# Kernel tuning notes

Measured on AMD Instinct MI355X. Metric: run time of the kernel, lower is better.

The kernel has to match this reference:

```python
import jax, jax.numpy as jnp
from jax import lax
import numpy as np

B, N, C = 16, 8192, 256


def farthest_point_sample(pts, npoint):
    # pts: [B, N, 3]. Standard PointNet++ FPS; is_center=True -> start from the
    # point farthest from the centroid (argmax of dist-to-mean).
    b, n, _ = pts.shape
    centroid = pts.mean(axis=1, keepdims=True)                  # [B,1,3]
    d0 = jnp.sum((pts - centroid) ** 2, axis=-1)                # [B,N]
    farthest = jnp.argmax(d0, axis=-1)                          # [B]
    dist = jnp.full((b, n), 1e10, dtype=pts.dtype)

    def step(carry, _):
        dist, far = carry
        cur = jnp.take_along_axis(pts, far[:, None, None], axis=1)  # [B,1,3]
        d = jnp.sum((pts - cur) ** 2, axis=-1)                      # [B,N]
        dist = jnp.minimum(dist, d)
        new_far = jnp.argmax(dist, axis=-1)
        return (dist, new_far), far

    (_, _), idxs = lax.scan(step, (dist, farthest), None, length=npoint)
    return idxs.T  # [B, npoint]


def index_points(x, idx):
    # x: [B, N, D], idx: [B, M] -> [B, M, D]
    return jnp.take_along_axis(x, idx[:, :, None], axis=1)


def setup_inputs() -> dict:
    key = jax.random.key(0)
    k1, k2 = jax.random.split(key)
    points = jax.random.normal(k1, (B, 3, N), dtype=jnp.float32)
    features = jax.random.normal(k2, (B, C, N), dtype=jnp.float32)
    return {"points": points, "features": features, "num_points": 2048}


def reference(points, features, num_points):
    pts = jnp.swapaxes(points, -1, -2)     # [B,N,3]
    feats = jnp.swapaxes(features, -1, -2) # [B,N,C]
    idx = farthest_point_sample(pts, num_points)  # [B,M] int
    sampled_points = index_points(pts, idx)       # [B,M,3]
    sampled_features = index_points(feats, idx)   # [B,M,C]
    return sampled_points, sampled_features
```

## Files before the change

### kernel.cpp

```cpp
#include <hip/hip_runtime.h>
#include <cfloat>

#define BB 16
#define NN 8192
#define CC 256
#define NT 256
#define PPT 32
#define NPAIR (PPT / 2)
#define NWAVES (NT / 64)
#define TIT (1024 / NT)
#define TBLOCKS 240
#define NTILES (BB * (CC / 64) * (NN / 64))

typedef float    v2f __attribute__((ext_vector_type(2)));
typedef unsigned v2u __attribute__((ext_vector_type(2)));
typedef unsigned uu;
typedef unsigned long long ull;

#define LDS_BARRIER() __asm__ __volatile__("s_waitcnt lgkmcnt(0)\n\ts_barrier" ::: "memory")

struct SmemFPS {
  float px[NN], py[NN], pz[NN];
  ull   key[2][NWAVES];
  float red[NWAVES][3];
  float ctr[3];
};
struct SmemT {
  float tile[64][65];
};
union Smem { SmemFPS f; SmemT t; };

__device__ __forceinline__ v2f pk_sub(v2f a, v2f b) {
  v2f d;
  asm("v_pk_add_f32 %0, %1, %2 neg_lo:[0,1] neg_hi:[0,1]"
      : "=v"(d) : "v"(a), "v"(b));
  return d;
}
__device__ __forceinline__ v2f pk_mul(v2f a, v2f b) {
  v2f d;
  asm("v_pk_mul_f32 %0, %1, %2" : "=v"(d) : "v"(a), "v"(b));
  return d;
}
__device__ __forceinline__ v2f pk_add(v2f a, v2f b) {
  v2f d;
  asm("v_pk_add_f32 %0, %1, %2" : "=v"(d) : "v"(a), "v"(b));
  return d;
}

__device__ __forceinline__ uu umin2(uu a, uu b) { return a < b ? a : b; }
__device__ __forceinline__ uu umax2(uu a, uu b) { return a > b ? a : b; }

__device__ __forceinline__ ull max64(ull a, ull b) { return a > b ? a : b; }

template <int CTRL>
__device__ __forceinline__ ull dpp_max64(ull x) {
  int lo = (int)(uu)x;
  int hi = (int)(uu)(x >> 32);
  int plo = __builtin_amdgcn_update_dpp(0, lo, CTRL, 0xF, 0xF, true);
  int phi = __builtin_amdgcn_update_dpp(0, hi, CTRL, 0xF, 0xF, true);
  ull p = ((ull)(uu)phi << 32) | (uu)plo;
  return max64(x, p);
}

__device__ __forceinline__ ull wave_max63(ull k) {
  k = dpp_max64<0xB1>(k);
  k = dpp_max64<0x4E>(k);
  k = dpp_max64<0x124>(k);
  k = dpp_max64<0x128>(k);
  k = dpp_max64<0x142>(k);
  k = dpp_max64<0x143>(k);
  return k;
}

__global__ __launch_bounds__(NT)
void fps_fused_kernel(const float* __restrict__ pts,
                      const float* __restrict__ feats,
                      float* __restrict__ out_pts,
                      int* __restrict__ idx_out,
                      float* __restrict__ trans, int M, int do_trans) {
  __shared__ Smem sm;
  const int t = threadIdx.x;

  if (blockIdx.x >= BB) {
    if (!do_trans) return;
    for (int tileId = blockIdx.x - BB; tileId < NTILES; tileId += TBLOCKS) {
      int b  = tileId / ((CC / 64) * (NN / 64));
      int r  = tileId % ((CC / 64) * (NN / 64));
      int ct = r / (NN / 64);
      int nt = r % (NN / 64);
      const float* src = feats + ((size_t)b * CC + ct * 64) * NN + nt * 64;
      float* dst = trans + ((size_t)b * NN + nt * 64) * CC + ct * 64;
#pragma unroll
      for (int i = 0; i < TIT; ++i) {
        int f = t + i * NT;
        int c = f >> 4, n4 = f & 15;
        float4 v = *(const float4*)(src + (size_t)c * NN + n4 * 4);
        sm.t.tile[c][n4 * 4 + 0] = v.x;
        sm.t.tile[c][n4 * 4 + 1] = v.y;
        sm.t.tile[c][n4 * 4 + 2] = v.z;
        sm.t.tile[c][n4 * 4 + 3] = v.w;
      }
      __syncthreads();
#pragma unroll
      for (int i = 0; i < TIT; ++i) {
        int f = t + i * NT;
        int n = f >> 4, c4 = f & 15;
        float4 o;
        o.x = sm.t.tile[c4 * 4 + 0][n];
        o.y = sm.t.tile[c4 * 4 + 1][n];
        o.z = sm.t.tile[c4 * 4 + 2][n];
        o.w = sm.t.tile[c4 * 4 + 3][n];
        *(float4*)(dst + (size_t)n * CC + c4 * 4) = o;
      }
      __syncthreads();
    }
    return;
  }

  const int b = blockIdx.x;
  const int wave = t >> 6;
  const int lane = t & 63;
  const float* base = pts + (size_t)b * 3 * NN;

  v2f px2[NPAIR], py2[NPAIR], pz2[NPAIR];
  v2u dist2[NPAIR];
  const uu INIT = __float_as_uint(1e10f);
#pragma unroll
  for (int j = 0; j < NPAIR; ++j) {
    int n0 = t + (2 * j) * NT;
    int n1 = t + (2 * j + 1) * NT;
    float x0 = base[n0], y0 = base[NN + n0], z0 = base[2 * NN + n0];
    float x1 = base[n1], y1 = base[NN + n1], z1 = base[2 * NN + n1];
    px2[j] = (v2f){x0, x1};
    py2[j] = (v2f){y0, y1};
    pz2[j] = (v2f){z0, z1};
    sm.f.px[n0] = x0; sm.f.py[n0] = y0; sm.f.pz[n0] = z0;
    sm.f.px[n1] = x1; sm.f.py[n1] = y1; sm.f.pz[n1] = z1;
    dist2[j] = (v2u){INIT, INIT};
  }

  float sx = 0.f, sy = 0.f, sz = 0.f;
#pragma unroll
  for (int j = 0; j < NPAIR; ++j) {
    sx += px2[j].x; sx += px2[j].y;
    sy += py2[j].x; sy += py2[j].y;
    sz += pz2[j].x; sz += pz2[j].y;
  }
#pragma unroll
  for (int off = 32; off > 0; off >>= 1) {
    sx += __shfl_xor(sx, off);
    sy += __shfl_xor(sy, off);
    sz += __shfl_xor(sz, off);
  }
  if (lane == 0) { sm.f.red[wave][0] = sx; sm.f.red[wave][1] = sy; sm.f.red[wave][2] = sz; }
  __syncthreads();
  if (t == 0) {
    float gx = 0.f, gy = 0.f, gz = 0.f;
    for (int w = 0; w < NWAVES; ++w) { gx += sm.f.red[w][0]; gy += sm.f.red[w][1]; gz += sm.f.red[w][2]; }
    sm.f.ctr[0] = gx / NN; sm.f.ctr[1] = gy / NN; sm.f.ctr[2] = gz / NN;
  }
  __syncthreads();
  const float ctx = sm.f.ctr[0], cty = sm.f.ctr[1], ctz = sm.f.ctr[2];

  int ep = 0;
  int ci;

  auto reduce_tail = [&](uu v, int bk) {
    ull key = ((ull)v << 32) | (uu)(~(uu)(t + bk * NT));
    key = wave_max63(key);
    ep ^= 1;
    if (lane == 63) sm.f.key[ep][wave] = key;
    LDS_BARRIER();
    ull kk = sm.f.key[ep][lane & 3];
    kk = dpp_max64<0xB1>(kk);
    kk = dpp_max64<0x4E>(kk);
    ci = (int)~(uu)kk;
  };

  {
    v2f c2x = {ctx, ctx}, c2y = {cty, cty}, c2z = {ctz, ctz};
    v2u nd2[NPAIR];
    uu v = 0u;
#pragma unroll
    for (int j = 0; j < NPAIR; ++j) {
      v2f dx = pk_sub(px2[j], c2x);
      v2f dy = pk_sub(py2[j], c2y);
      v2f dz = pk_sub(pz2[j], c2z);
      v2f d = pk_add(pk_add(pk_mul(dx, dx), pk_mul(dy, dy)), pk_mul(dz, dz));
      v2u du = (v2u){__float_as_uint(d.x), __float_as_uint(d.y)};
      nd2[j] = du;
      v = umax2(v, umax2(du.x, du.y));
    }
    int bk = 0;
#pragma unroll
    for (int k = PPT - 1; k >= 0; --k) {
      uu ndk = (k & 1) ? nd2[k >> 1].y : nd2[k >> 1].x;
      if (ndk == v) bk = k;
    }
    reduce_tail(v, bk);
  }

  for (int m = 0; m < M; ++m) {
    float cx = sm.f.px[ci], cy = sm.f.py[ci], cz = sm.f.pz[ci];
    if (t == 0) {
      idx_out[b * M + m] = ci;
      size_t o = ((size_t)b * M + m) * 3;
      out_pts[o] = cx; out_pts[o + 1] = cy; out_pts[o + 2] = cz;
    }
    if (m == M - 1) break;

    v2f c2x = {cx, cx}, c2y = {cy, cy}, c2z = {cz, cz};
    uu v = 0u;
#pragma unroll
    for (int j = 0; j < NPAIR; ++j) {
      v2f dx = pk_sub(px2[j], c2x);
      v2f dy = pk_sub(py2[j], c2y);
      v2f dz = pk_sub(pz2[j], c2z);
      v2f d = pk_add(pk_add(pk_mul(dx, dx), pk_mul(dy, dy)), pk_mul(dz, dz));
      v2u nd;
      nd.x = umin2(dist2[j].x, __float_as_uint(d.x));
      nd.y = umin2(dist2[j].y, __float_as_uint(d.y));
      dist2[j] = nd;
      v = umax2(v, umax2(nd.x, nd.y));
    }
    int bk = 0;
#pragma unroll
    for (int k = PPT - 1; k >= 0; --k) {
      uu ndk = (k & 1) ? dist2[k >> 1].y : dist2[k >> 1].x;
      if (ndk == v) bk = k;
    }
    reduce_tail(v, bk);
  }
}

__global__ __launch_bounds__(256)
void gather_t_kernel(const float* __restrict__ trans,
                     const int* __restrict__ idx,
                     float* __restrict__ out_f, int M) {
  int gm = blockIdx.x * 4 + (threadIdx.x >> 6);
  if (gm >= BB * M) return;
  int lane = threadIdx.x & 63;
  int b = gm / M;
  int n = idx[gm];
  float4 v = *(const float4*)(trans + ((size_t)b * NN + n) * CC + lane * 4);
  *(float4*)(out_f + (size_t)gm * CC + lane * 4) = v;
}

__global__ __launch_bounds__(CC)
void gather_kernel(const float* __restrict__ feats, const int* __restrict__ idx,
                   float* __restrict__ out_f, int M) {
  const int bm = blockIdx.x;
  const int b = bm / M;
  const int n = idx[bm];
  const int c = threadIdx.x;
  out_f[(size_t)bm * CC + c] = feats[((size_t)b * CC + c) * NN + n];
}

extern "C" void kernel_launch(void* const* d_in, const int* in_sizes, int n_in,
                              void* d_out, int out_size, void* d_ws, size_t ws_size,
                              hipStream_t stream) {
  const float* points = (const float*)d_in[0];
  const float* feats  = (const float*)d_in[1];
  int M = out_size / (BB * (3 + CC));
  if (M <= 0) M = 1;

  float* out_pts = (float*)d_out;
  float* out_f   = (float*)d_out + (size_t)BB * M * 3;

  int* idx_ws = (int*)d_ws;
  size_t idx_bytes = (((size_t)BB * M * sizeof(int)) + 255) & ~(size_t)255;
  size_t trans_bytes = (size_t)BB * NN * CC * sizeof(float);
  bool use_t = (ws_size >= idx_bytes + trans_bytes);
  float* trans = (float*)((char*)d_ws + idx_bytes);

  int grid = use_t ? (BB + TBLOCKS) : BB;
  fps_fused_kernel<<<dim3(grid), dim3(NT), 0, stream>>>(
      points, feats, out_pts, idx_ws, trans, M, use_t ? 1 : 0);

  if (use_t) {
    gather_t_kernel<<<dim3((BB * M + 3) / 4), dim3(256), 0, stream>>>(
        trans, idx_ws, out_f, M);
  } else {
    gather_kernel<<<dim3(BB * M), dim3(CC), 0, stream>>>(feats, idx_ws, out_f, M);
  }
}
```

Baseline: 2.027 ms.

## Carry winner coordinates through FPS argmax reduction and double threads per batch

The block size goes from 256 to 512 threads with 16 points per thread, and the per-point coordinate copies in shared memory are removed. Instead, each lane's argmax candidate carries its xyz through the DPP wave reduction and the cross-wave LDS stage, so the next centroid comes straight from registers rather than from a dependent LDS lookup. A tree-based select replaces the serial index scan. This shortens the per-iteration latency chain of the 2048-step serial loop, at the cost of moving three extra floats per DPP step and doing an 8-wave final reduction.

```diff
diff --git a/kernel.cpp b/kernel.cpp
--- a/kernel.cpp
+++ b/kernel.cpp
@@ -4,8 +4,8 @@
 #define BB 16
 #define NN 8192
 #define CC 256
-#define NT 256
-#define PPT 32
+#define NT 512
+#define PPT 16
 #define NPAIR (PPT / 2)
 #define NWAVES (NT / 64)
 #define TIT (1024 / NT)
@@ -20,10 +20,10 @@
 #define LDS_BARRIER() __asm__ __volatile__("s_waitcnt lgkmcnt(0)\n\ts_barrier" ::: "memory")
 
 struct SmemFPS {
-  float px[NN], py[NN], pz[NN];
-  ull   key[2][NWAVES];
-  float red[NWAVES][3];
-  float ctr[3];
+  ull    key[2][NWAVES];
+  float4 kc[2][NWAVES];
+  float  red[NWAVES][3];
+  float  ctr[3];
 };
 struct SmemT {
   float tile[64][65];
@@ -50,26 +50,21 @@
 __device__ __forceinline__ uu umin2(uu a, uu b) { return a < b ? a : b; }
 __device__ __forceinline__ uu umax2(uu a, uu b) { return a > b ? a : b; }
 
-__device__ __forceinline__ ull max64(ull a, ull b) { return a > b ? a : b; }
-
 template <int CTRL>
-__device__ __forceinline__ ull dpp_max64(ull x) {
-  int lo = (int)(uu)x;
-  int hi = (int)(uu)(x >> 32);
+__device__ __forceinline__ void dpp_step5(ull& k, float& x, float& y, float& z) {
+  int lo = (int)(uu)k;
+  int hi = (int)(uu)(k >> 32);
   int plo = __builtin_amdgcn_update_dpp(0, lo, CTRL, 0xF, 0xF, true);
   int phi = __builtin_amdgcn_update_dpp(0, hi, CTRL, 0xF, 0xF, true);
-  ull p = ((ull)(uu)phi << 32) | (uu)plo;
-  return max64(x, p);
-}
-
-__device__ __forceinline__ ull wave_max63(ull k) {
-  k = dpp_max64<0xB1>(k);
-  k = dpp_max64<0x4E>(k);
-  k = dpp_max64<0x124>(k);
-  k = dpp_max64<0x128>(k);
-  k = dpp_max64<0x142>(k);
-  k = dpp_max64<0x143>(k);
-  return k;
+  int pxi = __builtin_amdgcn_update_dpp(0, __float_as_int(x), CTRL, 0xF, 0xF, true);
+  int pyi = __builtin_amdgcn_update_dpp(0, __float_as_int(y), CTRL, 0xF, 0xF, true);
+  int pzi = __builtin_amdgcn_update_dpp(0, __float_as_int(z), CTRL, 0xF, 0xF, true);
+  ull pk = ((ull)(uu)phi << 32) | (uu)plo;
+  bool g = pk > k;
+  k = g ? pk : k;
+  x = g ? __int_as_float(pxi) : x;
+  y = g ? __int_as_float(pyi) : y;
+  z = g ? __int_as_float(pzi) : z;
 }
 
 __global__ __launch_bounds__(NT)
@@ -134,8 +129,6 @@
     px2[j] = (v2f){x0, x1};
     py2[j] = (v2f){y0, y1};
     pz2[j] = (v2f){z0, z1};
-    sm.f.px[n0] = x0; sm.f.py[n0] = y0; sm.f.pz[n0] = z0;
-    sm.f.px[n1] = x1; sm.f.py[n1] = y1; sm.f.pz[n1] = z1;
     dist2[j] = (v2u){INIT, INIT};
   }
 
@@ -163,18 +156,56 @@
   const float ctx = sm.f.ctr[0], cty = sm.f.ctr[1], ctz = sm.f.ctr[2];
 
   int ep = 0;
-  int ci;
-
-  auto reduce_tail = [&](uu v, int bk) {
-    ull key = ((ull)v << 32) | (uu)(~(uu)(t + bk * NT));
-    key = wave_max63(key);
+  int   wi;
+  float wx, wy, wz;
+
+  auto reduce_tail = [&](ull key, float kx, float ky, float kz) {
+    dpp_step5<0xB1>(key, kx, ky, kz);
+    dpp_step5<0x4E>(key, kx, ky, kz);
+    dpp_step5<0x124>(key, kx, ky, kz);
+    dpp_step5<0x128>(key, kx, ky, kz);
+    dpp_step5<0x142>(key, kx, ky, kz);
+    dpp_step5<0x143>(key, kx, ky, kz);
     ep ^= 1;
-    if (lane == 63) sm.f.key[ep][wave] = key;
+    if (lane == 63) {
+      sm.f.key[ep][wave] = key;
+      sm.f.kc[ep][wave] = make_float4(kx, ky, kz, 0.f);
+    }
     LDS_BARRIER();
-    ull kk = sm.f.key[ep][lane & 3];
-    kk = dpp_max64<0xB1>(kk);
-    kk = dpp_max64<0x4E>(kk);
-    ci = (int)~(uu)kk;
+    ull kk = sm.f.key[ep][lane & 7];
+    float4 cc = sm.f.kc[ep][lane & 7];
+    float bx = cc.x, by = cc.y, bz = cc.z;
+    dpp_step5<0xB1>(kk, bx, by, bz);
+    dpp_step5<0x4E>(kk, bx, by, bz);
+    dpp_step5<0x124>(kk, bx, by, bz);
+    wi = (int)~(uu)kk;
+    wx = bx; wy = by; wz = bz;
+  };
+
+  auto select_and_reduce = [&](uu v, const v2u* dd) {
+    uu bj[NPAIR]; float qx[NPAIR], qy[NPAIR], qz[NPAIR];
+#pragma unroll
+    for (int j = 0; j < NPAIR; ++j) {
+      bool c1 = (dd[j].x == v);
+      bool c2 = (dd[j].y == v);
+      bj[j] = c1 ? (uu)(2 * j) : (c2 ? (uu)(2 * j + 1) : 0xFFFFu);
+      qx[j] = c1 ? px2[j].x : px2[j].y;
+      qy[j] = c1 ? py2[j].x : py2[j].y;
+      qz[j] = c1 ? pz2[j].x : pz2[j].y;
+    }
+#pragma unroll
+    for (int s = 1; s < NPAIR; s <<= 1) {
+#pragma unroll
+      for (int j = 0; j + s < NPAIR; j += 2 * s) {
+        bool g = bj[j + s] < bj[j];
+        bj[j] = g ? bj[j + s] : bj[j];
+        qx[j] = g ? qx[j + s] : qx[j];
+        qy[j] = g ? qy[j + s] : qy[j];
+        qz[j] = g ? qz[j + s] : qz[j];
+      }
+    }
+    ull key = ((ull)v << 32) | (uu)(~(uu)(t + (int)bj[0] * NT));
+    reduce_tail(key, qx[0], qy[0], qz[0]);
   };
 
   {
@@ -191,19 +222,13 @@
       nd2[j] = du;
       v = umax2(v, umax2(du.x, du.y));
     }
-    int bk = 0;
-#pragma unroll
-    for (int k = PPT - 1; k >= 0; --k) {
-      uu ndk = (k & 1) ? nd2[k >> 1].y : nd2[k >> 1].x;
-      if (ndk == v) bk = k;
-    }
-    reduce_tail(v, bk);
+    select_and_reduce(v, nd2);
   }
 
   for (int m = 0; m < M; ++m) {
-    float cx = sm.f.px[ci], cy = sm.f.py[ci], cz = sm.f.pz[ci];
+    float cx = wx, cy = wy, cz = wz;
     if (t == 0) {
-      idx_out[b * M + m] = ci;
+      idx_out[b * M + m] = wi;
       size_t o = ((size_t)b * M + m) * 3;
       out_pts[o] = cx; out_pts[o + 1] = cy; out_pts[o + 2] = cz;
     }
@@ -223,13 +248,7 @@
       dist2[j] = nd;
       v = umax2(v, umax2(nd.x, nd.y));
     }
-    int bk = 0;
-#pragma unroll
-    for (int k = PPT - 1; k >= 0; --k) {
-      uu ndk = (k & 1) ? dist2[k >> 1].y : dist2[k >> 1].x;
-      if (ndk == v) bk = k;
-    }
-    reduce_tail(v, bk);
+    select_and_reduce(v, dist2);
   }
 }
 
```

Result: slower. 3.614 ms (+78.2%).

## Use 512 threads per FPS block and broadcast winner coordinates via LDS

Applied to the files above, without the earlier changes.

Each FPS block now runs 512 threads with 16 points per thread instead of 256 with 32, which halves the per-thread distance update loop but adds a wave to the cross-wave reduction. The full point cloud is no longer copied into shared memory. Instead, the lane holding each wave's maximum writes its key and its point's coordinates to LDS, and the final argmax's coordinates are broadcast with ballot and readlane. This removes the dependent indexed LDS load of the chosen point from each iteration's critical path. The cost is a runtime-indexed register select in the winning lane and a wider 8-wave final reduction.

```diff
diff --git a/kernel.cpp b/kernel.cpp
--- a/kernel.cpp
+++ b/kernel.cpp
@@ -4,8 +4,8 @@
 #define BB 16
 #define NN 8192
 #define CC 256
-#define NT 256
-#define PPT 32
+#define NT 512
+#define PPT 16
 #define NPAIR (PPT / 2)
 #define NWAVES (NT / 64)
 #define TIT (1024 / NT)
@@ -20,10 +20,10 @@
 #define LDS_BARRIER() __asm__ __volatile__("s_waitcnt lgkmcnt(0)\n\ts_barrier" ::: "memory")
 
 struct SmemFPS {
-  float px[NN], py[NN], pz[NN];
-  ull   key[2][NWAVES];
-  float red[NWAVES][3];
-  float ctr[3];
+  ull    key[2][NWAVES];
+  float4 kc[2][NWAVES];
+  float  red[NWAVES][3];
+  float  ctr[3];
 };
 struct SmemT {
   float tile[64][65];
@@ -70,6 +70,10 @@
   k = dpp_max64<0x142>(k);
   k = dpp_max64<0x143>(k);
   return k;
+}
+
+__device__ __forceinline__ float bcast_lane(float v, int src) {
+  return __int_as_float(__builtin_amdgcn_readlane(__float_as_int(v), src));
 }
 
 __global__ __launch_bounds__(NT)
@@ -134,8 +138,6 @@
     px2[j] = (v2f){x0, x1};
     py2[j] = (v2f){y0, y1};
     pz2[j] = (v2f){z0, z1};
-    sm.f.px[n0] = x0; sm.f.py[n0] = y0; sm.f.pz[n0] = z0;
-    sm.f.px[n1] = x1; sm.f.py[n1] = y1; sm.f.pz[n1] = z1;
     dist2[j] = (v2u){INIT, INIT};
   }
 
@@ -163,18 +165,42 @@
   const float ctx = sm.f.ctr[0], cty = sm.f.ctr[1], ctz = sm.f.ctr[2];
 
   int ep = 0;
-  int ci;
+  int   wi;
+  float wx, wy, wz;
 
   auto reduce_tail = [&](uu v, int bk) {
-    ull key = ((ull)v << 32) | (uu)(~(uu)(t + bk * NT));
-    key = wave_max63(key);
+    ull mykey = ((ull)v << 32) | (uu)(~(uu)(t + bk * NT));
+    ull k = wave_max63(mykey);
     ep ^= 1;
-    if (lane == 63) sm.f.key[ep][wave] = key;
+    uu wlo = (uu)__builtin_amdgcn_readlane((int)(uu)k, 63);
+    uu whi = (uu)__builtin_amdgcn_readlane((int)(uu)(k >> 32), 63);
+    ull wmax = ((ull)whi << 32) | wlo;
+    if (mykey == wmax) {
+      float qx = 0.f, qy = 0.f, qz = 0.f;
+#pragma unroll
+      for (int k2 = 0; k2 < PPT; ++k2) {
+        if (bk == k2) {
+          qx = (k2 & 1) ? px2[k2 >> 1].y : px2[k2 >> 1].x;
+          qy = (k2 & 1) ? py2[k2 >> 1].y : py2[k2 >> 1].x;
+          qz = (k2 & 1) ? pz2[k2 >> 1].y : pz2[k2 >> 1].x;
+        }
+      }
+      sm.f.key[ep][wave] = mykey;
+      sm.f.kc[ep][wave] = make_float4(qx, qy, qz, 0.f);
+    }
     LDS_BARRIER();
-    ull kk = sm.f.key[ep][lane & 3];
+    ull kk = sm.f.key[ep][lane & 7];
+    float4 cc = sm.f.kc[ep][lane & 7];
+    ull korig = kk;
     kk = dpp_max64<0xB1>(kk);
     kk = dpp_max64<0x4E>(kk);
-    ci = (int)~(uu)kk;
+    kk = dpp_max64<0x124>(kk);
+    wi = (int)~(uu)kk;
+    ull mm = __ballot(korig == kk);
+    int src = __ffsll((long long)mm) - 1;
+    wx = bcast_lane(cc.x, src);
+    wy = bcast_lane(cc.y, src);
+    wz = bcast_lane(cc.z, src);
   };
 
   {
@@ -201,9 +227,9 @@
   }
 
   for (int m = 0; m < M; ++m) {
-    float cx = sm.f.px[ci], cy = sm.f.py[ci], cz = sm.f.pz[ci];
+    float cx = wx, cy = wy, cz = wz;
     if (t == 0) {
-      idx_out[b * M + m] = ci;
+      idx_out[b * M + m] = wi;
       size_t o = ((size_t)b * M + m) * 3;
       out_pts[o] = cx; out_pts[o + 1] = cy; out_pts[o + 2] = cz;
     }
```

New measurement: 2.990 ms. 47.5% more time.

## Double FPS block threads, use packed 64-bit key tree reduction, prefetch winner coords

Applied to the files above, without the earlier changes.

Each FPS block now runs 512 threads with 16 points per thread instead of 256 threads with 32, which halves the per-thread serial work of each iteration. The per-thread argmax becomes a tree reduction over packed 64-bit (distance, inverted index) keys, replacing the max-then-scan-for-index pass. After the cross-wave LDS exchange, each lane reads the coordinates of its wave's candidate point before the final DPP reduction, and the winner's coordinates are taken with readlane, so the dependent LDS read at the start of the next iteration is gone. The cost is more waves taking part in each barrier, an 8-way instead of 4-way cross-wave reduce, and 64-bit compares in the per-thread tree.

```diff
diff --git a/kernel.cpp b/kernel.cpp
--- a/kernel.cpp
+++ b/kernel.cpp
@@ -4,8 +4,8 @@
 #define BB 16
 #define NN 8192
 #define CC 256
-#define NT 256
-#define PPT 32
+#define NT 512
+#define PPT 16
 #define NPAIR (PPT / 2)
 #define NWAVES (NT / 64)
 #define TIT (1024 / NT)
@@ -48,7 +48,6 @@
 }
 
 __device__ __forceinline__ uu umin2(uu a, uu b) { return a < b ? a : b; }
-__device__ __forceinline__ uu umax2(uu a, uu b) { return a > b ? a : b; }
 
 __device__ __forceinline__ ull max64(ull a, ull b) { return a > b ? a : b; }
 
@@ -71,6 +70,31 @@
   k = dpp_max64<0x143>(k);
   return k;
 }
+
+__device__ __forceinline__ float bcast_lane(float v, int src) {
+  return __int_as_float(__builtin_amdgcn_readlane(__float_as_int(v), src));
+}
+
+#define REDUCE_TAIL2(MYKEY)                                                    \
+  {                                                                            \
+    ull rt_w = wave_max63(MYKEY);                                              \
+    ep ^= 1;                                                                   \
+    if (lane == 63) sm.f.key[ep][wave] = rt_w;                                 \
+    LDS_BARRIER();                                                             \
+    ull rt_kk = sm.f.key[ep][lane & 7];                   \
+    uu rt_cand = ~(uu)rt_kk;                    \
+    float rt_qx = sm.f.px[rt_cand];            \
+    float rt_qy = sm.f.py[rt_cand];                                            \
+    float rt_qz = sm.f.pz[rt_cand];                                            \
+    rt_kk = dpp_max64<0xB1>(rt_kk);               \
+    rt_kk = dpp_max64<0x4E>(rt_kk);                                  \
+    rt_kk = dpp_max64<0x124>(rt_kk);               \
+    wi = (int)~(uu)rt_kk;                                                      \
+    int rt_src = (wi >> 6) & 7;                  \
+    wx = bcast_lane(rt_qx, rt_src);                                            \
+    wy = bcast_lane(rt_qy, rt_src);                                            \
+    wz = bcast_lane(rt_qz, rt_src);                                            \
+  }
 
 __global__ __launch_bounds__(NT)
 void fps_fused_kernel(const float* __restrict__ pts,
@@ -139,6 +163,10 @@
     dist2[j] = (v2u){INIT, INIT};
   }
 
+  uu ii[PPT];
+#pragma unroll
+  for (int k = 0; k < PPT; ++k) ii[k] = ~(uu)(t + k * NT);
+
   float sx = 0.f, sy = 0.f, sz = 0.f;
 #pragma unroll
   for (int j = 0; j < NPAIR; ++j) {
@@ -163,54 +191,40 @@
   const float ctx = sm.f.ctr[0], cty = sm.f.ctr[1], ctz = sm.f.ctr[2];
 
   int ep = 0;
-  int ci;
-
-  auto reduce_tail = [&](uu v, int bk) {
-    ull key = ((ull)v << 32) | (uu)(~(uu)(t + bk * NT));
-    key = wave_max63(key);
-    ep ^= 1;
-    if (lane == 63) sm.f.key[ep][wave] = key;
-    LDS_BARRIER();
-    ull kk = sm.f.key[ep][lane & 3];
-    kk = dpp_max64<0xB1>(kk);
-    kk = dpp_max64<0x4E>(kk);
-    ci = (int)~(uu)kk;
-  };
+  int   wi;
+  float wx, wy, wz;
 
   {
     v2f c2x = {ctx, ctx}, c2y = {cty, cty}, c2z = {ctz, ctz};
-    v2u nd2[NPAIR];
-    uu v = 0u;
+    ull kreg[PPT];
 #pragma unroll
     for (int j = 0; j < NPAIR; ++j) {
       v2f dx = pk_sub(px2[j], c2x);
       v2f dy = pk_sub(py2[j], c2y);
       v2f dz = pk_sub(pz2[j], c2z);
       v2f d = pk_add(pk_add(pk_mul(dx, dx), pk_mul(dy, dy)), pk_mul(dz, dz));
-      v2u du = (v2u){__float_as_uint(d.x), __float_as_uint(d.y)};
-      nd2[j] = du;
-      v = umax2(v, umax2(du.x, du.y));
-    }
-    int bk = 0;
-#pragma unroll
-    for (int k = PPT - 1; k >= 0; --k) {
-      uu ndk = (k & 1) ? nd2[k >> 1].y : nd2[k >> 1].x;
-      if (ndk == v) bk = k;
-    }
-    reduce_tail(v, bk);
+      kreg[2 * j]     = ((ull)__float_as_uint(d.x) << 32) | ii[2 * j];
+      kreg[2 * j + 1] = ((ull)__float_as_uint(d.y) << 32) | ii[2 * j + 1];
+    }
+#pragma unroll
+    for (int s = 1; s < PPT; s <<= 1) {
+#pragma unroll
+      for (int k = 0; k + s < PPT; k += 2 * s) kreg[k] = max64(kreg[k], kreg[k + s]);
+    }
+    REDUCE_TAIL2(kreg[0]);
   }
 
   for (int m = 0; m < M; ++m) {
-    float cx = sm.f.px[ci], cy = sm.f.py[ci], cz = sm.f.pz[ci];
+    float cx = wx, cy = wy, cz = wz;
     if (t == 0) {
-      idx_out[b * M + m] = ci;
+      idx_out[b * M + m] = wi;
       size_t o = ((size_t)b * M + m) * 3;
       out_pts[o] = cx; out_pts[o + 1] = cy; out_pts[o + 2] = cz;
     }
     if (m == M - 1) break;
 
     v2f c2x = {cx, cx}, c2y = {cy, cy}, c2z = {cz, cz};
-    uu v = 0u;
+    ull kreg[PPT];
 #pragma unroll
     for (int j = 0; j < NPAIR; ++j) {
       v2f dx = pk_sub(px2[j], c2x);
@@ -221,15 +235,15 @@
       nd.x = umin2(dist2[j].x, __float_as_uint(d.x));
       nd.y = umin2(dist2[j].y, __float_as_uint(d.y));
       dist2[j] = nd;
-      v = umax2(v, umax2(nd.x, nd.y));
-    }
-    int bk = 0;
-#pragma unroll
-    for (int k = PPT - 1; k >= 0; --k) {
-      uu ndk = (k & 1) ? dist2[k >> 1].y : dist2[k >> 1].x;
-      if (ndk == v) bk = k;
-    }
-    reduce_tail(v, bk);
+      kreg[2 * j]     = ((ull)nd.x << 32) | ii[2 * j];
+      kreg[2 * j + 1] = ((ull)nd.y << 32) | ii[2 * j + 1];
+    }
+#pragma unroll
+    for (int s = 1; s < PPT; s <<= 1) {
+#pragma unroll
+      for (int k = 0; k + s < PPT; k += 2 * s) kreg[k] = max64(kreg[k], kreg[k + s]);
+    }
+    REDUCE_TAIL2(kreg[0]);
   }
 }
 
```

Result: no change. 1.992 ms (-1.8%).
